# Optimization experiments

Hardware: AMD Instinct MI355X
Metric: run time of the kernel (lower is better)

The kernel has to match this reference:

```python
import jax, jax.numpy as jnp
import numpy as np

HIDDEN = 256
NUM_STEPS = 3
N_NODES = 200000
N_GRAPHS = 512


def setup_inputs() -> dict:
    key = jax.random.key(0)
    ks = jax.random.split(key, 8)
    h = HIDDEN
    x = jax.random.normal(ks[0], (N_NODES, h), dtype=jnp.float32)
    batch = jnp.sort(jax.random.randint(ks[1], (N_NODES,), 0, N_GRAPHS)).astype(jnp.int64)
    s_ih = 1.0 / np.sqrt(2 * h)
    s_hh = 1.0 / np.sqrt(h)
    # LSTM (input 2h -> hidden h), PyTorch gate order i,f,g,o
    W_ih = jax.random.uniform(ks[2], (4 * h, 2 * h), jnp.float32, -s_ih, s_ih)
    W_hh = jax.random.uniform(ks[3], (4 * h, h), jnp.float32, -s_hh, s_hh)
    b_ih = jax.random.uniform(ks[4], (4 * h,), jnp.float32, -s_hh, s_hh)
    b_hh = jax.random.uniform(ks[5], (4 * h,), jnp.float32, -s_hh, s_hh)
    # out_proj: Linear(2h -> h)
    s_o = 1.0 / np.sqrt(2 * h)
    W_out = jax.random.uniform(ks[6], (h, 2 * h), jnp.float32, -s_o, s_o)
    b_out = jax.random.uniform(ks[7], (h,), jnp.float32, -s_o, s_o)
    return {"x": x, "batch": batch, "W_ih": W_ih, "W_hh": W_hh,
            "b_ih": b_ih, "b_hh": b_hh, "W_out": W_out, "b_out": b_out,
            "n_graphs": N_GRAPHS}


def _set2set(x, batch, W_ih, W_hh, b_ih, b_hh, n_graphs):
    h = x.shape[1]
    hs = jnp.zeros((n_graphs, h), x.dtype)
    cs = jnp.zeros((n_graphs, h), x.dtype)
    q_star = jnp.zeros((n_graphs, 2 * h), x.dtype)
    for _ in range(NUM_STEPS):
        # LSTM step (PyTorch gate order: i, f, g, o)
        gates = q_star @ W_ih.T + hs @ W_hh.T + (b_ih + b_hh)  # [B, 4h]
        i_g, f_g, g_g, o_g = jnp.split(gates, 4, axis=-1)
        cs = jax.nn.sigmoid(f_g) * cs + jax.nn.sigmoid(i_g) * jnp.tanh(g_g)
        hs = jax.nn.sigmoid(o_g) * jnp.tanh(cs)
        q = hs  # [B, h]
        # attention logits per node
        e = jnp.sum(x * q[batch], axis=-1)  # [N]
        # segment softmax over nodes of each graph
        m = jax.ops.segment_max(e, batch, num_segments=n_graphs)
        a = jnp.exp(e - m[batch])
        denom = jax.ops.segment_sum(a, batch, num_segments=n_graphs)
        a = a / denom[batch]
        # weighted readout
        r = jax.ops.segment_sum(a[:, None] * x, batch, num_segments=n_graphs)  # [B, h]
        q_star = jnp.concatenate([q, r], axis=-1)  # [B, 2h]
    return q_star


def reference(x, batch, W_ih, W_hh, b_ih, b_hh, W_out, b_out, n_graphs):
    q_star = _set2set(x, batch.astype(jnp.int32), W_ih, W_hh, b_ih, b_hh, n_graphs)
    return q_star @ W_out.T + b_out
```

## Files before the change

kernel.cpp:

```cpp
#include <hip/hip_runtime.h>
#include <hip/hip_bf16.h>

#define HID 256
#define NG 512

__device__ __forceinline__ float sigmoidf_(float v) { return 1.f / (1.f + __expf(-v)); }

__global__ __launch_bounds__(256) void prep_kernel(
    const float* __restrict__ W_ih, const float* __restrict__ W_hh,
    const float* __restrict__ b_ih, const float* __restrict__ b_hh,
    const int* __restrict__ batch, int n,
    float* __restrict__ Wcat, float* __restrict__ bcat, int* __restrict__ starts)
{
    int b = blockIdx.x, tid = threadIdx.x;
    if (b < 512) {
        int o = (b * 256 + tid) * 4;
        int k = o & 511, row = o >> 9;
        float4 v = *(const float4*)&W_ih[o];
        if (k < 256) {
            float4 u = *(const float4*)&W_hh[row * 256 + k];
            v.x += u.x; v.y += u.y; v.z += u.z; v.w += u.w;
        }
        *(float4*)&Wcat[o] = v;
    } else if (b < 516) {
        int i = (b - 512) * 256 + tid;
        bcat[i] = b_ih[i] + b_hh[i];
    } else {
        int g = (b - 516) * 256 + tid;
        if (g > NG) return;
        if (g == NG) { starts[NG] = n; return; }
        int lo = 0, hi = n;
        while (lo < hi) {
            int mid = (lo + hi) >> 1;
            if (batch[mid] < g) lo = mid + 1; else hi = mid;
        }
        starts[g] = lo;
    }
}

__global__ __launch_bounds__(256) void attn_kernel(
    const float* __restrict__ x, const int* __restrict__ starts,
    const float* __restrict__ gp, const float* __restrict__ bcat,
    float* __restrict__ cs, float* __restrict__ qs, int step0)
{
    __shared__ __align__(16) float ql[HID];
    __shared__ __align__(16) float red[4][HID];
    __shared__ float mw[4], lw[4];

    const int g = blockIdx.x;
    const int tid = threadIdx.x;

    float ig, fg, gg, og;
    if (step0) {
        ig = bcat[tid]; fg = bcat[256 + tid]; gg = bcat[512 + tid]; og = bcat[768 + tid];
    } else {
        const float* a0 = gp + (size_t)g * 1024;
        const float* a1 = a0 + (size_t)512 * 1024;
        ig = a0[tid]       + a1[tid]       + bcat[tid];
        fg = a0[256 + tid] + a1[256 + tid] + bcat[256 + tid];
        gg = a0[512 + tid] + a1[512 + tid] + bcat[512 + tid];
        og = a0[768 + tid] + a1[768 + tid] + bcat[768 + tid];
    }
    float cp = step0 ? 0.f : cs[g * HID + tid];
    float cn = sigmoidf_(fg) * cp + sigmoidf_(ig) * tanhf(gg);
    float h  = sigmoidf_(og) * tanhf(cn);
    cs[g * HID + tid] = cn;
    qs[(size_t)g * 512 + tid] = h;
    ql[tid] = h;

    const int s0 = starts[g];
    const int nn = starts[g + 1] - s0;
    if (nn <= 0) { qs[(size_t)g * 512 + HID + tid] = 0.f; return; }
    __syncthreads();

    const int w = tid >> 6, lane = tid & 63;
    const float4 qv = *(const float4*)&ql[lane * 4];
    const float* xg = x + (size_t)s0 * HID + lane * 4;
    const int lastrow = nn - 1;
    const float NEG = -3.402823466e38f;

    float m_run = NEG, l_run = 0.f;
    float4 racc = make_float4(0.f, 0.f, 0.f, 0.f);
    float4 y0, y1, y2, y3, z0, z1, z2, z3;

    int row0 = 4 * w;
    if (row0 < nn) {
        int r1 = row0 + 1 > lastrow ? lastrow : row0 + 1;
        int r2 = row0 + 2 > lastrow ? lastrow : row0 + 2;
        int r3 = row0 + 3 > lastrow ? lastrow : row0 + 3;
        y0 = *(const float4*)(xg + (size_t)row0 * HID);
        y1 = *(const float4*)(xg + (size_t)r1 * HID);
        y2 = *(const float4*)(xg + (size_t)r2 * HID);
        y3 = *(const float4*)(xg + (size_t)r3 * HID);
    }
    for (; row0 < nn; row0 += 16) {
        const int nr = row0 + 16;
        if (nr < nn) {
            int r1 = nr + 1 > lastrow ? lastrow : nr + 1;
            int r2 = nr + 2 > lastrow ? lastrow : nr + 2;
            int r3 = nr + 3 > lastrow ? lastrow : nr + 3;
            z0 = *(const float4*)(xg + (size_t)nr * HID);
            z1 = *(const float4*)(xg + (size_t)r1 * HID);
            z2 = *(const float4*)(xg + (size_t)r2 * HID);
            z3 = *(const float4*)(xg + (size_t)r3 * HID);
        }
        float d0 = y0.x * qv.x + y0.y * qv.y + y0.z * qv.z + y0.w * qv.w;
        float d1 = y1.x * qv.x + y1.y * qv.y + y1.z * qv.z + y1.w * qv.w;
        float d2 = y2.x * qv.x + y2.y * qv.y + y2.z * qv.z + y2.w * qv.w;
        float d3 = y3.x * qv.x + y3.y * qv.y + y3.z * qv.z + y3.w * qv.w;
        #pragma unroll
        for (int off = 1; off < 64; off <<= 1) {
            d0 += __shfl_xor(d0, off);
            d1 += __shfl_xor(d1, off);
            d2 += __shfl_xor(d2, off);
            d3 += __shfl_xor(d3, off);
        }
        const float e0 = d0;
        const float e1 = (row0 + 1 < nn) ? d1 : NEG;
        const float e2 = (row0 + 2 < nn) ? d2 : NEG;
        const float e3 = (row0 + 3 < nn) ? d3 : NEG;
        const float em = fmaxf(fmaxf(e0, e1), fmaxf(e2, e3));
        if (em > m_run) {
            const float alpha = __expf(m_run - em);
            const float p0 = __expf(e0 - em);
            const float p1 = __expf(e1 - em);
            const float p2 = __expf(e2 - em);
            const float p3 = __expf(e3 - em);
            l_run = l_run * alpha + (p0 + p1) + (p2 + p3);
            racc.x = racc.x * alpha + p0 * y0.x + p1 * y1.x + p2 * y2.x + p3 * y3.x;
            racc.y = racc.y * alpha + p0 * y0.y + p1 * y1.y + p2 * y2.y + p3 * y3.y;
            racc.z = racc.z * alpha + p0 * y0.z + p1 * y1.z + p2 * y2.z + p3 * y3.z;
            racc.w = racc.w * alpha + p0 * y0.w + p1 * y1.w + p2 * y2.w + p3 * y3.w;
            m_run = em;
        } else {
            const float p0 = __expf(e0 - m_run);
            const float p1 = __expf(e1 - m_run);
            const float p2 = __expf(e2 - m_run);
            const float p3 = __expf(e3 - m_run);
            l_run += (p0 + p1) + (p2 + p3);
            racc.x += p0 * y0.x + p1 * y1.x + p2 * y2.x + p3 * y3.x;
            racc.y += p0 * y0.y + p1 * y1.y + p2 * y2.y + p3 * y3.y;
            racc.z += p0 * y0.z + p1 * y1.z + p2 * y2.z + p3 * y3.z;
            racc.w += p0 * y0.w + p1 * y1.w + p2 * y2.w + p3 * y3.w;
        }
        y0 = z0; y1 = z1; y2 = z2; y3 = z3;
    }

    *(float4*)&red[w][lane * 4] = racc;
    if (lane == 0) { mw[w] = m_run; lw[w] = l_run; }
    __syncthreads();
    const float M = fmaxf(fmaxf(mw[0], mw[1]), fmaxf(mw[2], mw[3]));
    const float f0 = __expf(mw[0] - M), f1 = __expf(mw[1] - M);
    const float f2 = __expf(mw[2] - M), f3 = __expf(mw[3] - M);
    const float L = lw[0] * f0 + lw[1] * f1 + lw[2] * f2 + lw[3] * f3;
    const float r = red[0][tid] * f0 + red[1][tid] * f1
                  + red[2][tid] * f2 + red[3][tid] * f3;
    qs[(size_t)g * 512 + HID + tid] = r / L;
}

__global__ __launch_bounds__(256) void gemm_splitk(
    const float* __restrict__ A, int lda,
    const float* __restrict__ B, int ldb,
    float* __restrict__ Cp, int ldc, int KS, size_t slice_stride)
{
    __shared__ float As[16][76];
    __shared__ float Bs[16][76];
    const int tid = threadIdx.x;
    const int tx = tid & 15, ty = tid >> 4;
    const int m0 = blockIdx.y * 64, n0 = blockIdx.x * 64;
    const int kb = blockIdx.z * KS;
    const int r = tid >> 2, kc = (tid & 3) << 2;
    float acc[4][4] = {};

    const float* Ap = &A[(size_t)(m0 + r) * lda + kb + kc];
    const float* Bp = &B[(size_t)(n0 + r) * ldb + kb + kc];
    float4 av = *(const float4*)Ap;
    float4 bv = *(const float4*)Bp;

    for (int k0 = 0; k0 < KS; k0 += 16) {
        As[kc + 0][r] = av.x; As[kc + 1][r] = av.y; As[kc + 2][r] = av.z; As[kc + 3][r] = av.w;
        Bs[kc + 0][r] = bv.x; Bs[kc + 1][r] = bv.y; Bs[kc + 2][r] = bv.z; Bs[kc + 3][r] = bv.w;
        __syncthreads();
        if (k0 + 16 < KS) {
            av = *(const float4*)(Ap + k0 + 16);
            bv = *(const float4*)(Bp + k0 + 16);
        }
        #pragma unroll
        for (int kk = 0; kk < 16; ++kk) {
            float4 a = *(const float4*)&As[kk][ty << 2];
            float4 b = *(const float4*)&Bs[kk][tx << 2];
            acc[0][0] += a.x * b.x; acc[0][1] += a.x * b.y; acc[0][2] += a.x * b.z; acc[0][3] += a.x * b.w;
            acc[1][0] += a.y * b.x; acc[1][1] += a.y * b.y; acc[1][2] += a.y * b.z; acc[1][3] += a.y * b.w;
            acc[2][0] += a.z * b.x; acc[2][1] += a.z * b.y; acc[2][2] += a.z * b.z; acc[2][3] += a.z * b.w;
            acc[3][0] += a.w * b.x; acc[3][1] += a.w * b.y; acc[3][2] += a.w * b.z; acc[3][3] += a.w * b.w;
        }
        __syncthreads();
    }
    float* out = Cp + blockIdx.z * slice_stride;
    #pragma unroll
    for (int i = 0; i < 4; ++i) {
        float4 o = make_float4(acc[i][0], acc[i][1], acc[i][2], acc[i][3]);
        *(float4*)&out[(size_t)(m0 + ty * 4 + i) * ldc + n0 + (tx << 2)] = o;
    }
}

__global__ __launch_bounds__(256) void finalize_out(
    const float* __restrict__ op, const float* __restrict__ b_out,
    float* __restrict__ out)
{
    int i = blockIdx.x * 256 + threadIdx.x;
    if (i < 512 * 256) {
        out[i] = op[i] + op[131072 + i] + op[262144 + i] + op[393216 + i] + b_out[i & 255];
    }
}

extern "C" void kernel_launch(void* const* d_in, const int* in_sizes, int n_in,
                              void* d_out, int out_size, void* d_ws, size_t ws_size,
                              hipStream_t stream)
{
    const float* x     = (const float*)d_in[0];
    const int*   batch = (const int*)d_in[1];
    const float* W_ih  = (const float*)d_in[2];
    const float* W_hh  = (const float*)d_in[3];
    const float* b_ih  = (const float*)d_in[4];
    const float* b_hh  = (const float*)d_in[5];
    const float* W_out = (const float*)d_in[6];
    const float* b_out = (const float*)d_in[7];
    float* out = (float*)d_out;
    const int n = in_sizes[1];
    (void)n_in; (void)out_size; (void)ws_size;

    char* ws = (char*)d_ws;
    float* qs     = (float*)(ws);
    float* cs     = (float*)(ws + 0x100000);
    float* gp     = (float*)(ws + 0x180000);
    float* Wcat   = (float*)(ws + 0x580000);
    float* bcat   = (float*)(ws + 0x780000);
    int*   starts = (int*)  (ws + 0x781000);
    float* op     = (float*)(ws + 0x790000);

    prep_kernel<<<519, 256, 0, stream>>>(W_ih, W_hh, b_ih, b_hh, batch, n,
                                         Wcat, bcat, starts);
    for (int step = 0; step < 3; ++step) {
        if (step > 0) {
            gemm_splitk<<<dim3(16, 8, 2), 256, 0, stream>>>(
                qs, 512, Wcat, 512, gp, 1024, 256, (size_t)512 * 1024);
        }
        attn_kernel<<<NG, 256, 0, stream>>>(x, starts, gp, bcat, cs, qs, step == 0);
    }
    gemm_splitk<<<dim3(4, 8, 4), 256, 0, stream>>>(
        qs, 512, W_out, 512, op, 256, 128, (size_t)512 * 256);
    finalize_out<<<512, 256, 0, stream>>>(op, b_out, out);
}
```

Baseline: 413.5 us.

## Fuse whole Set2Set pipeline into one cooperative persistent kernel with grid syncs

Replaces the sequence of prep, split-K GEMM, attention and finalize launches with a single cooperative kernel of 256 blocks × 512 threads. Each block runs two independent 256-thread halves, and the stages are separated by grid.sync(). LSTM cell state is kept in registers across steps, and the split-K factor rises to 4 for the gate GEMM and 16 for the output GEMM so the fixed grid is filled. This removes launch overhead and inter-kernel gaps. In exchange it runs the bandwidth-bound attention pass with only 256 resident blocks, and adds grid-barrier cost plus more partial-sum traffic.

```diff
diff --git a/kernel.cpp b/kernel.cpp
--- a/kernel.cpp
+++ b/kernel.cpp
@@ -1,10 +1,249 @@
 #include <hip/hip_runtime.h>
 #include <hip/hip_bf16.h>
+#include <hip/hip_cooperative_groups.h>
+
+namespace cg = cooperative_groups;
 
 #define HID 256
 #define NG 512
 
 __device__ __forceinline__ float sigmoidf_(float v) { return 1.f / (1.f + __expf(-v)); }
+
+struct SM {
+    float As[16][76];
+    float Bs[16][76];
+    float ql[HID];
+    float red[4][HID];
+    float mw[4], lw[4];
+};
+
+__device__ __forceinline__ void gemm_tile(
+    const float* __restrict__ A, int lda, const float* __restrict__ B, int ldb,
+    float* __restrict__ C, int ldc, int m0, int n0, int kb, int KS,
+    SM& sm, int ltid)
+{
+    const int tx = ltid & 15, ty = ltid >> 4;
+    const int r = ltid >> 2, kc = (ltid & 3) << 2;
+    float acc[4][4] = {};
+    const float* Ap = &A[(size_t)(m0 + r) * lda + kb + kc];
+    const float* Bp = &B[(size_t)(n0 + r) * ldb + kb + kc];
+    float4 av = *(const float4*)Ap;
+    float4 bv = *(const float4*)Bp;
+    for (int k0 = 0; k0 < KS; k0 += 16) {
+        sm.As[kc + 0][r] = av.x; sm.As[kc + 1][r] = av.y;
+        sm.As[kc + 2][r] = av.z; sm.As[kc + 3][r] = av.w;
+        sm.Bs[kc + 0][r] = bv.x; sm.Bs[kc + 1][r] = bv.y;
+        sm.Bs[kc + 2][r] = bv.z; sm.Bs[kc + 3][r] = bv.w;
+        __syncthreads();
+        if (k0 + 16 < KS) {
+            av = *(const float4*)(Ap + k0 + 16);
+            bv = *(const float4*)(Bp + k0 + 16);
+        }
+        #pragma unroll
+        for (int kk = 0; kk < 16; ++kk) {
+            float4 a  = *(const float4*)&sm.As[kk][ty << 2];
+            float4 b4 = *(const float4*)&sm.Bs[kk][tx << 2];
+            acc[0][0] += a.x * b4.x; acc[0][1] += a.x * b4.y; acc[0][2] += a.x * b4.z; acc[0][3] += a.x * b4.w;
+            acc[1][0] += a.y * b4.x; acc[1][1] += a.y * b4.y; acc[1][2] += a.y * b4.z; acc[1][3] += a.y * b4.w;
+            acc[2][0] += a.z * b4.x; acc[2][1] += a.z * b4.y; acc[2][2] += a.z * b4.z; acc[2][3] += a.z * b4.w;
+            acc[3][0] += a.w * b4.x; acc[3][1] += a.w * b4.y; acc[3][2] += a.w * b4.z; acc[3][3] += a.w * b4.w;
+        }
+        __syncthreads();
+    }
+    #pragma unroll
+    for (int i = 0; i < 4; ++i) {
+        float4 o = make_float4(acc[i][0], acc[i][1], acc[i][2], acc[i][3]);
+        *(float4*)&C[(size_t)(m0 + ty * 4 + i) * ldc + n0 + (tx << 2)] = o;
+    }
+}
+
+__device__ __forceinline__ void attn_graph_half(
+    const float* __restrict__ x, const int* __restrict__ starts,
+    const float* __restrict__ gp, const float* __restrict__ bcat,
+    float* __restrict__ qs, float& cstate, int g, int ltid, int step0, SM& sm)
+{
+    float ig, fg, gg, og;
+    ig = bcat[ltid]; fg = bcat[256 + ltid]; gg = bcat[512 + ltid]; og = bcat[768 + ltid];
+    if (!step0) {
+        const float* a0 = gp + (size_t)g * 1024;
+        #pragma unroll
+        for (int z = 0; z < 4; ++z) {
+            const float* az = a0 + (size_t)z * 512 * 1024;
+            ig += az[ltid]; fg += az[256 + ltid]; gg += az[512 + ltid]; og += az[768 + ltid];
+        }
+    }
+    float cp = step0 ? 0.f : cstate;
+    float cn = sigmoidf_(fg) * cp + sigmoidf_(ig) * tanhf(gg);
+    float h  = sigmoidf_(og) * tanhf(cn);
+    cstate = cn;
+    qs[(size_t)g * 512 + ltid] = h;
+    sm.ql[ltid] = h;
+
+    const int s0 = starts[g];
+    const int nn = starts[g + 1] - s0;
+    __syncthreads();
+
+    const int w = ltid >> 6, lane = ltid & 63;
+    const float NEG = -3.402823466e38f;
+    float m_run = NEG, l_run = 0.f;
+    float4 racc = make_float4(0.f, 0.f, 0.f, 0.f);
+
+    if (nn > 0) {
+        const float4 qv = *(const float4*)&sm.ql[lane * 4];
+        const float* xg = x + (size_t)s0 * HID + lane * 4;
+        const int lastrow = nn - 1;
+        float4 y0, y1, y2, y3, z0, z1, z2, z3;
+
+        int row0 = 4 * w;
+        if (row0 < nn) {
+            int r1 = row0 + 1 > lastrow ? lastrow : row0 + 1;
+            int r2 = row0 + 2 > lastrow ? lastrow : row0 + 2;
+            int r3 = row0 + 3 > lastrow ? lastrow : row0 + 3;
+            y0 = *(const float4*)(xg + (size_t)row0 * HID);
+            y1 = *(const float4*)(xg + (size_t)r1 * HID);
+            y2 = *(const float4*)(xg + (size_t)r2 * HID);
+            y3 = *(const float4*)(xg + (size_t)r3 * HID);
+        }
+        for (; row0 < nn; row0 += 16) {
+            const int nr = row0 + 16;
+            if (nr < nn) {
+                int r1 = nr + 1 > lastrow ? lastrow : nr + 1;
+                int r2 = nr + 2 > lastrow ? lastrow : nr + 2;
+                int r3 = nr + 3 > lastrow ? lastrow : nr + 3;
+                z0 = *(const float4*)(xg + (size_t)nr * HID);
+                z1 = *(const float4*)(xg + (size_t)r1 * HID);
+                z2 = *(const float4*)(xg + (size_t)r2 * HID);
+                z3 = *(const float4*)(xg + (size_t)r3 * HID);
+            }
+            float d0 = y0.x * qv.x + y0.y * qv.y + y0.z * qv.z + y0.w * qv.w;
+            float d1 = y1.x * qv.x + y1.y * qv.y + y1.z * qv.z + y1.w * qv.w;
+            float d2 = y2.x * qv.x + y2.y * qv.y + y2.z * qv.z + y2.w * qv.w;
+            float d3 = y3.x * qv.x + y3.y * qv.y + y3.z * qv.z + y3.w * qv.w;
+            #pragma unroll
+            for (int off = 1; off < 64; off <<= 1) {
+                d0 += __shfl_xor(d0, off);
+                d1 += __shfl_xor(d1, off);
+                d2 += __shfl_xor(d2, off);
+                d3 += __shfl_xor(d3, off);
+            }
+            const float e0 = d0;
+            const float e1 = (row0 + 1 < nn) ? d1 : NEG;
+            const float e2 = (row0 + 2 < nn) ? d2 : NEG;
+            const float e3 = (row0 + 3 < nn) ? d3 : NEG;
+            const float em = fmaxf(fmaxf(e0, e1), fmaxf(e2, e3));
+            if (em > m_run) {
+                const float alpha = __expf(m_run - em);
+                const float p0 = __expf(e0 - em);
+                const float p1 = __expf(e1 - em);
+                const float p2 = __expf(e2 - em);
+                const float p3 = __expf(e3 - em);
+                l_run = l_run * alpha + (p0 + p1) + (p2 + p3);
+                racc.x = racc.x * alpha + p0 * y0.x + p1 * y1.x + p2 * y2.x + p3 * y3.x;
+                racc.y = racc.y * alpha + p0 * y0.y + p1 * y1.y + p2 * y2.y + p3 * y3.y;
+                racc.z = racc.z * alpha + p0 * y0.z + p1 * y1.z + p2 * y2.z + p3 * y3.z;
+                racc.w = racc.w * alpha + p0 * y0.w + p1 * y1.w + p2 * y2.w + p3 * y3.w;
+                m_run = em;
+            } else {
+                const float p0 = __expf(e0 - m_run);
+                const float p1 = __expf(e1 - m_run);
+                const float p2 = __expf(e2 - m_run);
+                const float p3 = __expf(e3 - m_run);
+                l_run += (p0 + p1) + (p2 + p3);
+                racc.x += p0 * y0.x + p1 * y1.x + p2 * y2.x + p3 * y3.x;
+                racc.y += p0 * y0.y + p1 * y1.y + p2 * y2.y + p3 * y3.y;
+                racc.z += p0 * y0.z + p1 * y1.z + p2 * y2.z + p3 * y3.z;
+                racc.w += p0 * y0.w + p1 * y1.w + p2 * y2.w + p3 * y3.w;
+            }
+            y0 = z0; y1 = z1; y2 = z2; y3 = z3;
+        }
+    }
+    *(float4*)&sm.red[w][lane * 4] = racc;
+    if (lane == 0) { sm.mw[w] = m_run; sm.lw[w] = l_run; }
+    __syncthreads();
+
+    float rout = 0.f;
+    if (nn > 0) {
+        const float M = fmaxf(fmaxf(sm.mw[0], sm.mw[1]), fmaxf(sm.mw[2], sm.mw[3]));
+        const float f0 = __expf(sm.mw[0] - M), f1 = __expf(sm.mw[1] - M);
+        const float f2 = __expf(sm.mw[2] - M), f3 = __expf(sm.mw[3] - M);
+        const float L = sm.lw[0] * f0 + sm.lw[1] * f1 + sm.lw[2] * f2 + sm.lw[3] * f3;
+        rout = (sm.red[0][ltid] * f0 + sm.red[1][ltid] * f1
+              + sm.red[2][ltid] * f2 + sm.red[3][ltid] * f3) / L;
+    }
+    qs[(size_t)g * 512 + HID + ltid] = rout;
+}
+
+__global__ __launch_bounds__(512, 2) void fused_kernel(
+    const float* __restrict__ x, const int* __restrict__ batch,
+    const float* __restrict__ W_ih, const float* __restrict__ W_hh,
+    const float* __restrict__ b_ih, const float* __restrict__ b_hh,
+    const float* __restrict__ W_out, const float* __restrict__ b_out,
+    float* __restrict__ out, int n, char* __restrict__ ws)
+{
+    __shared__ SM sm2[2];
+    float* qs     = (float*)(ws);
+    float* gp     = (float*)(ws + 0x100000);
+    float* Wcat   = (float*)(ws + 0x900000);
+    float* bcat   = (float*)(ws + 0xB00000);
+    int*   starts = (int*)  (ws + 0xB01000);
+    float* op     = (float*)(ws + 0xB10000);
+
+    cg::grid_group grid = cg::this_grid();
+    const int b = blockIdx.x, tid = threadIdx.x;
+    const int hf = tid >> 8, ltid = tid & 255;
+    const int htask = b * 2 + hf;
+    const int gtid = b * 512 + tid;
+    SM& sm = sm2[hf];
+
+    {
+        int o = gtid * 4;
+        int k = o & 511, row = o >> 9;
+        float4 v = *(const float4*)&W_ih[o];
+        if (k < 256) {
+            float4 u = *(const float4*)&W_hh[row * 256 + k];
+            v.x += u.x; v.y += u.y; v.z += u.z; v.w += u.w;
+        }
+        *(float4*)&Wcat[o] = v;
+    }
+    if (gtid < 1024) bcat[gtid] = b_ih[gtid] + b_hh[gtid];
+    if (gtid <= NG) {
+        if (gtid == NG) starts[NG] = n;
+        else {
+            int lo = 0, hi = n;
+            while (lo < hi) {
+                int mid = (lo + hi) >> 1;
+                if (batch[mid] < gtid) lo = mid + 1; else hi = mid;
+            }
+            starts[gtid] = lo;
+        }
+    }
+    grid.sync();
+
+    float cstate = 0.f;
+    for (int step = 0; step < 3; ++step) {
+        if (step > 0) {
+            int bz = htask >> 7, rem = htask & 127;
+            gemm_tile(qs, 512, Wcat, 512, gp + (size_t)bz * 512 * 1024, 1024,
+                      (rem >> 4) * 64, (rem & 15) * 64, bz * 128, 128, sm, ltid);
+            grid.sync();
+        }
+        attn_graph_half(x, starts, gp, bcat, qs, cstate, htask, ltid, step == 0, sm);
+        grid.sync();
+    }
+
+    {
+        int bz = htask >> 5, rem = htask & 31;
+        gemm_tile(qs, 512, W_out, 512, op + (size_t)bz * 512 * 256, 256,
+                  (rem >> 2) * 64, (rem & 3) * 64, bz * 32, 32, sm, ltid);
+    }
+    grid.sync();
+    {
+        float v = b_out[gtid & 255];
+        #pragma unroll
+        for (int z = 0; z < 16; ++z) v += op[(size_t)z * 131072 + gtid];
+        out[gtid] = v;
+    }
+}
 
 __global__ __launch_bounds__(256) void prep_kernel(
     const float* __restrict__ W_ih, const float* __restrict__ W_hh,
@@ -43,119 +282,111 @@
     const float* __restrict__ gp, const float* __restrict__ bcat,
     float* __restrict__ cs, float* __restrict__ qs, int step0)
 {
-    __shared__ __align__(16) float ql[HID];
-    __shared__ __align__(16) float red[4][HID];
-    __shared__ float mw[4], lw[4];
-
-    const int g = blockIdx.x;
-    const int tid = threadIdx.x;
-
-    float ig, fg, gg, og;
-    if (step0) {
-        ig = bcat[tid]; fg = bcat[256 + tid]; gg = bcat[512 + tid]; og = bcat[768 + tid];
-    } else {
+    __shared__ SM sm;
+    const int g = blockIdx.x, tid = threadIdx.x;
+    float dummy_c = 0.f;
+    float cprev = step0 ? 0.f : cs[g * HID + tid];
+    (void)dummy_c;
+    float ig = bcat[tid], fg = bcat[256 + tid], gg = bcat[512 + tid], og = bcat[768 + tid];
+    if (!step0) {
         const float* a0 = gp + (size_t)g * 1024;
-        const float* a1 = a0 + (size_t)512 * 1024;
-        ig = a0[tid]       + a1[tid]       + bcat[tid];
-        fg = a0[256 + tid] + a1[256 + tid] + bcat[256 + tid];
-        gg = a0[512 + tid] + a1[512 + tid] + bcat[512 + tid];
-        og = a0[768 + tid] + a1[768 + tid] + bcat[768 + tid];
-    }
-    float cp = step0 ? 0.f : cs[g * HID + tid];
-    float cn = sigmoidf_(fg) * cp + sigmoidf_(ig) * tanhf(gg);
+        #pragma unroll
+        for (int z = 0; z < 4; ++z) {
+            const float* az = a0 + (size_t)z * 512 * 1024;
+            ig += az[tid]; fg += az[256 + tid]; gg += az[512 + tid]; og += az[768 + tid];
+        }
+    }
+    float cn = sigmoidf_(fg) * cprev + sigmoidf_(ig) * tanhf(gg);
     float h  = sigmoidf_(og) * tanhf(cn);
     cs[g * HID + tid] = cn;
+    float cst = cn;
     qs[(size_t)g * 512 + tid] = h;
-    ql[tid] = h;
-
+    sm.ql[tid] = h;
     const int s0 = starts[g];
     const int nn = starts[g + 1] - s0;
-    if (nn <= 0) { qs[(size_t)g * 512 + HID + tid] = 0.f; return; }
     __syncthreads();
-
     const int w = tid >> 6, lane = tid & 63;
-    const float4 qv = *(const float4*)&ql[lane * 4];
-    const float* xg = x + (size_t)s0 * HID + lane * 4;
-    const int lastrow = nn - 1;
     const float NEG = -3.402823466e38f;
-
     float m_run = NEG, l_run = 0.f;
     float4 racc = make_float4(0.f, 0.f, 0.f, 0.f);
-    float4 y0, y1, y2, y3, z0, z1, z2, z3;
-
-    int row0 = 4 * w;
-    if (row0 < nn) {
-        int r1 = row0 + 1 > lastrow ? lastrow : row0 + 1;
-        int r2 = row0 + 2 > lastrow ? lastrow : row0 + 2;
-        int r3 = row0 + 3 > lastrow ? lastrow : row0 + 3;
-        y0 = *(const float4*)(xg + (size_t)row0 * HID);
-        y1 = *(const float4*)(xg + (size_t)r1 * HID);
-        y2 = *(const float4*)(xg + (size_t)r2 * HID);
-        y3 = *(const float4*)(xg + (size_t)r3 * HID);
-    }
-    for (; row0 < nn; row0 += 16) {
-        const int nr = row0 + 16;
-        if (nr < nn) {
-            int r1 = nr + 1 > lastrow ? lastrow : nr + 1;
-            int r2 = nr + 2 > lastrow ? lastrow : nr + 2;
-            int r3 = nr + 3 > lastrow ? lastrow : nr + 3;
-            z0 = *(const float4*)(xg + (size_t)nr * HID);
-            z1 = *(const float4*)(xg + (size_t)r1 * HID);
-            z2 = *(const float4*)(xg + (size_t)r2 * HID);
-            z3 = *(const float4*)(xg + (size_t)r3 * HID);
-        }
-        float d0 = y0.x * qv.x + y0.y * qv.y + y0.z * qv.z + y0.w * qv.w;
-        float d1 = y1.x * qv.x + y1.y * qv.y + y1.z * qv.z + y1.w * qv.w;
-        float d2 = y2.x * qv.x + y2.y * qv.y + y2.z * qv.z + y2.w * qv.w;
-        float d3 = y3.x * qv.x + y3.y * qv.y + y3.z * qv.z + y3.w * qv.w;
-        #pragma unroll
-        for (int off = 1; off < 64; off <<= 1) {
-            d0 += __shfl_xor(d0, off);
-            d1 += __shfl_xor(d1, off);
-            d2 += __shfl_xor(d2, off);
-            d3 += __shfl_xor(d3, off);
-        }
-        const float e0 = d0;
-        const float e1 = (row0 + 1 < nn) ? d1 : NEG;
-        const float e2 = (row0 + 2 < nn) ? d2 : NEG;
-        const float e3 = (row0 + 3 < nn) ? d3 : NEG;
-        const float em = fmaxf(fmaxf(e0, e1), fmaxf(e2, e3));
-        if (em > m_run) {
-            const float alpha = __expf(m_run - em);
-            const float p0 = __expf(e0 - em);
-            const float p1 = __expf(e1 - em);
-            const float p2 = __expf(e2 - em);
-            const float p3 = __expf(e3 - em);
-            l_run = l_run * alpha + (p0 + p1) + (p2 + p3);
-            racc.x = racc.x * alpha + p0 * y0.x + p1 * y1.x + p2 * y2.x + p3 * y3.x;
-            racc.y = racc.y * alpha + p0 * y0.y + p1 * y1.y + p2 * y2.y + p3 * y3.y;
-            racc.z = racc.z * alpha + p0 * y0.z + p1 * y1.z + p2 * y2.z + p3 * y3.z;
-            racc.w = racc.w * alpha + p0 * y0.w + p1 * y1.w + p2 * y2.w + p3 * y3.w;
-            m_run = em;
-        } else {
-            const float p0 = __expf(e0 - m_run);
-            const float p1 = __expf(e1 - m_run);
-            const float p2 = __expf(e2 - m_run);
-            const float p3 = __expf(e3 - m_run);
-            l_run += (p0 + p1) + (p2 + p3);
-            racc.x += p0 * y0.x + p1 * y1.x + p2 * y2.x + p3 * y3.x;
-            racc.y += p0 * y0.y + p1 * y1.y + p2 * y2.y + p3 * y3.y;
-            racc.z += p0 * y0.z + p1 * y1.z + p2 * y2.z + p3 * y3.z;
-            racc.w += p0 * y0.w + p1 * y1.w + p2 * y2.w + p3 * y3.w;
-        }
-        y0 = z0; y1 = z1; y2 = z2; y3 = z3;
-    }
-
-    *(float4*)&red[w][lane * 4] = racc;
-    if (lane == 0) { mw[w] = m_run; lw[w] = l_run; }
+    if (nn > 0) {
+        const float4 qv = *(const float4*)&sm.ql[lane * 4];
+        const float* xg = x + (size_t)s0 * HID + lane * 4;
+        const int lastrow = nn - 1;
+        float4 y0, y1, y2, y3, z0, z1, z2, z3;
+        int row0 = 4 * w;
+        if (row0 < nn) {
+            int r1 = row0 + 1 > lastrow ? lastrow : row0 + 1;
+            int r2 = row0 + 2 > lastrow ? lastrow : row0 + 2;
+            int r3 = row0 + 3 > lastrow ? lastrow : row0 + 3;
+            y0 = *(const float4*)(xg + (size_t)row0 * HID);
+            y1 = *(const float4*)(xg + (size_t)r1 * HID);
+            y2 = *(const float4*)(xg + (size_t)r2 * HID);
+            y3 = *(const float4*)(xg + (size_t)r3 * HID);
+        }
+        for (; row0 < nn; row0 += 16) {
+            const int nr = row0 + 16;
+            if (nr < nn) {
+                int r1 = nr + 1 > lastrow ? lastrow : nr + 1;
+                int r2 = nr + 2 > lastrow ? lastrow : nr + 2;
+                int r3 = nr + 3 > lastrow ? lastrow : nr + 3;
+                z0 = *(const float4*)(xg + (size_t)nr * HID);
+                z1 = *(const float4*)(xg + (size_t)r1 * HID);
+                z2 = *(const float4*)(xg + (size_t)r2 * HID);
+                z3 = *(const float4*)(xg + (size_t)r3 * HID);
+            }
+            float d0 = y0.x * qv.x + y0.y * qv.y + y0.z * qv.z + y0.w * qv.w;
+            float d1 = y1.x * qv.x + y1.y * qv.y + y1.z * qv.z + y1.w * qv.w;
+            float d2 = y2.x * qv.x + y2.y * qv.y + y2.z * qv.z + y2.w * qv.w;
+            float d3 = y3.x * qv.x + y3.y * qv.y + y3.z * qv.z + y3.w * qv.w;
+            #pragma unroll
+            for (int off = 1; off < 64; off <<= 1) {
+                d0 += __shfl_xor(d0, off);
+                d1 += __shfl_xor(d1, off);
+                d2 += __shfl_xor(d2, off);
+                d3 += __shfl_xor(d3, off);
+            }
+            const float e0 = d0;
+            const float e1 = (row0 + 1 < nn) ? d1 : NEG;
+            const float e2 = (row0 + 2 < nn) ? d2 : NEG;
+            const float e3 = (row0 + 3 < nn) ? d3 : NEG;
+            const float em = fmaxf(fmaxf(e0, e1), fmaxf(e2, e3));
+            if (em > m_run) {
+                const float alpha = __expf(m_run - em);
+                const float p0 = __expf(e0 - em), p1 = __expf(e1 - em);
+                const float p2 = __expf(e2 - em), p3 = __expf(e3 - em);
+                l_run = l_run * alpha + (p0 + p1) + (p2 + p3);
+                racc.x = racc.x * alpha + p0 * y0.x + p1 * y1.x + p2 * y2.x + p3 * y3.x;
+                racc.y = racc.y * alpha + p0 * y0.y + p1 * y1.y + p2 * y2.y + p3 * y3.y;
+                racc.z = racc.z * alpha + p0 * y0.z + p1 * y1.z + p2 * y2.z + p3 * y3.z;
+                racc.w = racc.w * alpha + p0 * y0.w + p1 * y1.w + p2 * y2.w + p3 * y3.w;
+                m_run = em;
+            } else {
+                const float p0 = __expf(e0 - m_run), p1 = __expf(e1 - m_run);
+                const float p2 = __expf(e2 - m_run), p3 = __expf(e3 - m_run);
+                l_run += (p0 + p1) + (p2 + p3);
+                racc.x += p0 * y0.x + p1 * y1.x + p2 * y2.x + p3 * y3.x;
+                racc.y += p0 * y0.y + p1 * y1.y + p2 * y2.y + p3 * y3.y;
+                racc.z += p0 * y0.z + p1 * y1.z + p2 * y2.z + p3 * y3.z;
+                racc.w += p0 * y0.w + p1 * y1.w + p2 * y2.w + p3 * y3.w;
+            }
+            y0 = z0; y1 = z1; y2 = z2; y3 = z3;
+        }
+    }
+    (void)cst;
+    *(float4*)&sm.red[w][lane * 4] = racc;
+    if (lane == 0) { sm.mw[w] = m_run; sm.lw[w] = l_run; }
     __syncthreads();
-    const float M = fmaxf(fmaxf(mw[0], mw[1]), fmaxf(mw[2], mw[3]));
-    const float f0 = __expf(mw[0] - M), f1 = __expf(mw[1] - M);
-    const float f2 = __expf(mw[2] - M), f3 = __expf(mw[3] - M);
-    const float L = lw[0] * f0 + lw[1] * f1 + lw[2] * f2 + lw[3] * f3;
-    const float r = red[0][tid] * f0 + red[1][tid] * f1
-                  + red[2][tid] * f2 + red[3][tid] * f3;
-    qs[(size_t)g * 512 + HID + tid] = r / L;
+    float rout = 0.f;
+    if (nn > 0) {
+        const float M = fmaxf(fmaxf(sm.mw[0], sm.mw[1]), fmaxf(sm.mw[2], sm.mw[3]));
+        const float f0 = __expf(sm.mw[0] - M), f1 = __expf(sm.mw[1] - M);
+        const float f2 = __expf(sm.mw[2] - M), f3 = __expf(sm.mw[3] - M);
+        const float L = sm.lw[0] * f0 + sm.lw[1] * f1 + sm.lw[2] * f2 + sm.lw[3] * f3;
+        rout = (sm.red[0][tid] * f0 + sm.red[1][tid] * f1
+              + sm.red[2][tid] * f2 + sm.red[3][tid] * f3) / L;
+    }
+    qs[(size_t)g * 512 + HID + tid] = rout;
 }
 
 __global__ __launch_bounds__(256) void gemm_splitk(
@@ -163,45 +394,10 @@
     const float* __restrict__ B, int ldb,
     float* __restrict__ Cp, int ldc, int KS, size_t slice_stride)
 {
-    __shared__ float As[16][76];
-    __shared__ float Bs[16][76];
-    const int tid = threadIdx.x;
-    const int tx = tid & 15, ty = tid >> 4;
-    const int m0 = blockIdx.y * 64, n0 = blockIdx.x * 64;
-    const int kb = blockIdx.z * KS;
-    const int r = tid >> 2, kc = (tid & 3) << 2;
-    float acc[4][4] = {};
-
-    const float* Ap = &A[(size_t)(m0 + r) * lda + kb + kc];
-    const float* Bp = &B[(size_t)(n0 + r) * ldb + kb + kc];
-    float4 av = *(const float4*)Ap;
-    float4 bv = *(const float4*)Bp;
-
-    for (int k0 = 0; k0 < KS; k0 += 16) {
-        As[kc + 0][r] = av.x; As[kc + 1][r] = av.y; As[kc + 2][r] = av.z; As[kc + 3][r] = av.w;
-        Bs[kc + 0][r] = bv.x; Bs[kc + 1][r] = bv.y; Bs[kc + 2][r] = bv.z; Bs[kc + 3][r] = bv.w;
-        __syncthreads();
-        if (k0 + 16 < KS) {
-            av = *(const float4*)(Ap + k0 + 16);
-            bv = *(const float4*)(Bp + k0 + 16);
-        }
-        #pragma unroll
-        for (int kk = 0; kk < 16; ++kk) {
-            float4 a = *(const float4*)&As[kk][ty << 2];
-            float4 b = *(const float4*)&Bs[kk][tx << 2];
-            acc[0][0] += a.x * b.x; acc[0][1] += a.x * b.y; acc[0][2] += a.x * b.z; acc[0][3] += a.x * b.w;
-            acc[1][0] += a.y * b.x; acc[1][1] += a.y * b.y; acc[1][2] += a.y * b.z; acc[1][3] += a.y * b.w;
-            acc[2][0] += a.z * b.x; acc[2][1] += a.z * b.y; acc[2][2] += a.z * b.z; acc[2][3] += a.z * b.w;
-            acc[3][0] += a.w * b.x; acc[3][1] += a.w * b.y; acc[3][2] += a.w * b.z; acc[3][3] += a.w * b.w;
-        }
-        __syncthreads();
-    }
-    float* out = Cp + blockIdx.z * slice_stride;
-    #pragma unroll
-    for (int i = 0; i < 4; ++i) {
-        float4 o = make_float4(acc[i][0], acc[i][1], acc[i][2], acc[i][3]);
-        *(float4*)&out[(size_t)(m0 + ty * 4 + i) * ldc + n0 + (tx << 2)] = o;
-    }
+    __shared__ SM sm;
+    gemm_tile(A, lda, B, ldb, Cp + blockIdx.z * slice_stride, ldc,
+              blockIdx.y * 64, blockIdx.x * 64, blockIdx.z * KS, KS,
+              sm, threadIdx.x);
 }
 
 __global__ __launch_bounds__(256) void finalize_out(
@@ -209,9 +405,10 @@
     float* __restrict__ out)
 {
     int i = blockIdx.x * 256 + threadIdx.x;
-    if (i < 512 * 256) {
-        out[i] = op[i] + op[131072 + i] + op[262144 + i] + op[393216 + i] + b_out[i & 255];
-    }
+    float v = b_out[i & 255];
+    #pragma unroll
+    for (int z = 0; z < 4; ++z) v += op[(size_t)z * 131072 + i];
+    out[i] = v;
 }
 
 extern "C" void kernel_launch(void* const* d_in, const int* in_sizes, int n_in,
@@ -227,24 +424,31 @@
     const float* W_out = (const float*)d_in[6];
     const float* b_out = (const float*)d_in[7];
     float* out = (float*)d_out;
-    const int n = in_sizes[1];
+    int n = in_sizes[1];
+    char* ws = (char*)d_ws;
     (void)n_in; (void)out_size; (void)ws_size;
 
-    char* ws = (char*)d_ws;
+    void* args[] = { (void*)&x, (void*)&batch, (void*)&W_ih, (void*)&W_hh,
+                     (void*)&b_ih, (void*)&b_hh, (void*)&W_out, (void*)&b_out,
+                     (void*)&out, (void*)&n, (void*)&ws };
+    hipError_t rc = hipLaunchCooperativeKernel((const void*)fused_kernel,
+                                               dim3(256), dim3(512), args, 0, stream);
+    if (rc == hipSuccess) return;
+
     float* qs     = (float*)(ws);
-    float* cs     = (float*)(ws + 0x100000);
-    float* gp     = (float*)(ws + 0x180000);
-    float* Wcat   = (float*)(ws + 0x580000);
-    float* bcat   = (float*)(ws + 0x780000);
-    int*   starts = (int*)  (ws + 0x781000);
-    float* op     = (float*)(ws + 0x790000);
+    float* gp     = (float*)(ws + 0x100000);
+    float* Wcat   = (float*)(ws + 0x900000);
+    float* bcat   = (float*)(ws + 0xB00000);
+    int*   starts = (int*)  (ws + 0xB01000);
+    float* op     = (float*)(ws + 0xB10000);
+    float* cs     = (float*)(ws + 0xD10000);
 
     prep_kernel<<<519, 256, 0, stream>>>(W_ih, W_hh, b_ih, b_hh, batch, n,
                                          Wcat, bcat, starts);
     for (int step = 0; step < 3; ++step) {
         if (step > 0) {
-            gemm_splitk<<<dim3(16, 8, 2), 256, 0, stream>>>(
-                qs, 512, Wcat, 512, gp, 1024, 256, (size_t)512 * 1024);
+            gemm_splitk<<<dim3(16, 8, 4), 256, 0, stream>>>(
+                qs, 512, Wcat, 512, gp, 1024, 128, (size_t)512 * 1024);
         }
         attn_kernel<<<NG, 256, 0, stream>>>(x, starts, gp, bcat, cs, qs, step == 0);
     }
```

After: 616.7 us. 1.49x slower.
